# Kernel tuning notes

Hardware: AMD Instinct MI355X
Metric: run time of the kernel (lower is better)

The kernel has to match this reference:

```python
import jax, jax.numpy as jnp
import numpy as np

B, T = 64, 64
H = 256
CLIP = 0.2


def _conv(x, W, b, s):
    y = jax.lax.conv_general_dilated(x, W, (s, s), 'VALID',
                                     dimension_numbers=('NHWC', 'HWIO', 'NHWC'))
    return jax.nn.leaky_relu(y + b, negative_slope=0.2)


def _lstm(x, Wk, Wr, b):
    # keras LSTM, gate order i,f,g,o; x: (B,T,256) -> (B,T,256)
    h0 = jnp.zeros((x.shape[0], H), x.dtype)

    def step(carry, xt):
        h, c = carry
        z = xt @ Wk + h @ Wr + b
        i, f, g, o = jnp.split(z, 4, axis=-1)
        c = jax.nn.sigmoid(f) * c + jax.nn.sigmoid(i) * jnp.tanh(g)
        h = jax.nn.sigmoid(o) * jnp.tanh(c)
        return (h, c), h

    _, hs = jax.lax.scan(step, (h0, h0), jnp.swapaxes(x, 0, 1))
    return jnp.swapaxes(hs, 0, 1)


def setup_inputs():
    key = jax.random.key(0)
    ks = jax.random.split(key, 24)
    s = 0.05
    x = jax.random.normal(ks[0], (B, T, 13, 8, 8), jnp.float32)
    a_taken = jax.random.randint(ks[1], (B, T), 0, 36)
    mask = jax.random.randint(ks[2], (B, T, 4096), 0, 2).astype(jnp.int32)
    # taken actions must be legal (mask=1), as in real rollouts
    bi = jnp.repeat(jnp.arange(B), T)
    ti = jnp.tile(jnp.arange(T), B)
    mask = mask.at[bi, ti, a_taken.reshape(-1)].set(1)
    lg_prob_old = -jnp.abs(jax.random.normal(ks[3], (B, T), jnp.float32)) - 1.0
    GAE = jax.random.normal(ks[4], (B, T), jnp.float32)
    old_v_pred = jax.random.normal(ks[5], (B, T), jnp.float32)
    returns = jax.random.normal(ks[6], (B, T), jnp.float32)
    return {
        'x': x, 'mask': mask, 'lg_prob_old': lg_prob_old, 'a_taken': a_taken,
        'GAE': GAE, 'old_v_pred': old_v_pred, 'returns': returns,
        'W1': jax.random.normal(ks[7], (2, 2, 8, 16), jnp.float32) * s,
        'b1': jnp.zeros((16,), jnp.float32),
        'W2': jax.random.normal(ks[8], (2, 2, 16, 32), jnp.float32) * s,
        'b2': jnp.zeros((32,), jnp.float32),
        'W3': jax.random.normal(ks[9], (2, 2, 32, 64), jnp.float32) * s,
        'b3': jnp.zeros((64,), jnp.float32),
        'W4': jax.random.normal(ks[10], (1, 1, 64, 128), jnp.float32) * s,
        'b4': jnp.zeros((128,), jnp.float32),
        'lstm_k': jax.random.normal(ks[11], (256, 1024), jnp.float32) * s,
        'lstm_r': jax.random.normal(ks[12], (256, 1024), jnp.float32) * s,
        'lstm_b': jnp.zeros((1024,), jnp.float32),
        'pir_W': jax.random.normal(ks[13], (256, 36), jnp.float32) * s,
        'pir_b': jnp.zeros((36,), jnp.float32),
        'pim_W': jax.random.normal(ks[14], (256, 4096), jnp.float32) * s,
        'pim_b': jnp.zeros((4096,), jnp.float32),
        'v_W': jax.random.normal(ks[15], (256, 1), jnp.float32) * s,
        'v_b': jnp.zeros((1,), jnp.float32),
    }


def reference(x, mask, lg_prob_old, a_taken, GAE, old_v_pred, returns,
              W1, b1, W2, b2, W3, b3, W4, b4,
              lstm_k, lstm_r, lstm_b, pir_W, pir_b, pim_W, pim_b, v_W, v_b):
    Bn, Tn = x.shape[0], x.shape[1]
    h = x.reshape(Bn * Tn, 13, 8, 8)  # NHWC: H=13, W=8, C=8
    h = _conv(h, W1, b1, 2)  # (BT,6,4,16)
    h = _conv(h, W2, b2, 1)  # (BT,5,3,32)
    h = _conv(h, W3, b3, 2)  # (BT,2,1,64)
    h = _conv(h, W4, b4, 1)  # (BT,2,1,128)
    # keras Flatten(data_format='channels_first') permutes dim1 to last then flattens
    h = jnp.transpose(h, (0, 2, 3, 1)).reshape(Bn, Tn, -1)  # (B,T,256)
    lstm = _lstm(h, lstm_k, lstm_r, lstm_b).reshape(-1, H)  # (BT,256)

    pir = jax.nn.softmax(lstm @ pir_W + pir_b, axis=-1)  # (BT,36)
    maskf = mask.reshape(-1, 4096).astype(jnp.float32)
    pim = jax.nn.softmax(lstm @ pim_W + pim_b, axis=-1) * maskf
    scale = jnp.sum(pim, axis=1, keepdims=True)
    pim = pim / jnp.where(scale > 0, scale, jnp.ones_like(scale))  # (BT,4096)
    vpred = lstm @ v_W + v_b  # (BT,1)

    lg_old = lg_prob_old.reshape(-1)
    a = a_taken.reshape(-1)
    gae = GAE.reshape(-1)
    ovp = old_v_pred.reshape(-1)
    ret = returns.reshape(-1)
    gae = (gae - jnp.mean(gae)) / (jnp.std(gae) + 1e-8)

    t = jnp.arange(a.shape[0])
    p = jnp.where(t % 2 == 0, pir[t, a], pim[t, a])  # alternating heads
    lg_new = jnp.log(p)
    rt = jnp.exp(lg_new - lg_old)
    pg1 = -gae * rt
    pg2 = -gae * jnp.clip(rt, 1.0 - CLIP, 1.0 + CLIP)
    pg_loss = jnp.mean(jnp.maximum(pg1, pg2))

    # faithful to original TF: (BT,1) vpred broadcast against (BT,) -> (BT,BT)
    vpredclipped = ovp + jnp.clip(vpred - ovp, -CLIP, CLIP)
    vf1 = jnp.square(vpred - ret)
    vf2 = jnp.square(vpredclipped - ret)
    vf_loss = 0.5 * jnp.mean(jnp.maximum(vf1, vf2))

    pim_e = pim + (1.0 - maskf)
    entropy = -jnp.sum(pir * jnp.log(pir)) - jnp.sum(pim_e * jnp.log(pim_e))
    loss = pg_loss - entropy + vf_loss
    return (loss, pg_loss, entropy, vf_loss)
```

## Files before the change

### kernel.cpp

```cpp
#include <hip/hip_runtime.h>

typedef unsigned short u16;
typedef unsigned int   u32;

#define BT   4096
#define TSEQ 64
#define NB   64

typedef __attribute__((ext_vector_type(8))) short  short8;
typedef __attribute__((ext_vector_type(4))) float  f32x4;
typedef __attribute__((ext_vector_type(2))) _Float16 h2;

__device__ __forceinline__ float bf(u16 v) {
    u32 u = ((u32)v) << 16;
    return __builtin_bit_cast(float, u);
}
__device__ __forceinline__ u16 f2b(float f) {
    u32 u = __builtin_bit_cast(u32, f);
    return (u16)((u + 0x7fffu + ((u >> 16) & 1u)) >> 16);
}
__device__ __forceinline__ float lrelu(float x) { return x > 0.f ? x : 0.2f * x; }
__device__ __forceinline__ h2 i2h(int v) { return __builtin_bit_cast(h2, v); }
__device__ __forceinline__ float dot2(int hbits, int wbits, float acc) {
#if __has_builtin(__builtin_amdgcn_fdot2)
    return __builtin_amdgcn_fdot2(i2h(hbits), i2h(wbits), acc, false);
#else
    h2 a = i2h(hbits), b = i2h(wbits);
    return acc + (float)a.x * (float)b.x + (float)a.y * (float)b.y;
#endif
}
__device__ __forceinline__ float fsigm(float x) { return 1.f / (1.f + __expf(-x)); }
__device__ __forceinline__ float ftanh(float x) { return 1.f - 2.f / (__expf(2.f * x) + 1.f); }
__device__ __forceinline__ float ldf(const void* p, int i, int f32) {
    return f32 ? ((const float*)p)[i] : bf(((const u16*)p)[i]);
}
__device__ __forceinline__ u16 ldb(const void* p, int i, int f32) {
    return f32 ? f2b(((const float*)p)[i]) : ((const u16*)p)[i];
}

struct PrepPtrs {
    const void *x, *W1, *b1, *W2, *b2, *W3, *b3, *W4, *b4;
    const void *Wr, *Wk, *Wpim, *Wpir, *Wv;
    const u16* probe;
    u16 *featbf, *PF, *PBk, *PBpim, *PBpir;
    float* scal; int* flag;
};

#define PACK_BLKS 776
#define CONV_BLKS 2048

__global__ __launch_bounds__(256) void prep_kernel(PrepPtrs P)
{
    const int bid = blockIdx.x, tid = threadIdx.x;
    const int lane = tid & 63;
    u16 pv = P.probe[2 * lane];
    int e = (pv >> 7) & 0xFF;
    unsigned long long m = __ballot(pv == 0 || (e >= 100 && e <= 130));
    const int f32 = (__popcll(m) < 48) ? 1 : 0;

    if (bid == 0 && tid < 32) { P.scal[tid] = 0.f; if (tid == 0) *P.flag = f32; }

    if (bid < PACK_BLKS) {
        u16 t8[8];
        if (bid < 128) {
            int gid = bid * 256 + tid;
            int col = gid & 1023, oct = gid >> 10;
#pragma unroll
            for (int j = 0; j < 8; j++) {
                float f = ldf(P.Wr, (oct * 8 + j) * 1024 + col, f32);
                _Float16 h = (_Float16)f;
                t8[j] = __builtin_bit_cast(unsigned short, h);
            }
            *(int4*)&P.PF[((size_t)oct * 1024 + col) * 8] = *(int4*)t8;
        } else if (bid < 256) {
            int gid = (bid - 128) * 256 + tid;
            int col = gid & 1023, oct = gid >> 10;
#pragma unroll
            for (int j = 0; j < 8; j++) t8[j] = ldb(P.Wk, (oct * 8 + j) * 1024 + col, f32);
            *(int4*)&P.PBk[((((size_t)(oct >> 2) << 10) + col) * 4 + (oct & 3)) * 8] = *(int4*)t8;
        } else if (bid < 768) {
            int gid = (bid - 256) * 256 + tid;
            int col = gid & 4095, oct = gid >> 12;
#pragma unroll
            for (int j = 0; j < 8; j++) t8[j] = ldb(P.Wpim, (size_t)(oct * 8 + j) * 4096 + col, f32);
            *(int4*)&P.PBpim[((((size_t)(oct >> 2) << 12) + col) * 4 + (oct & 3)) * 8] = *(int4*)t8;
        } else {
            int gid = (bid - 768) * 256 + tid;
            int col = gid & 63, oct = gid >> 6;
#pragma unroll
            for (int j = 0; j < 8; j++) {
                int k = oct * 8 + j;
                u16 v = 0;
                if (col < 36)       v = ldb(P.Wpir, k * 36 + col, f32);
                else if (col == 36) v = ldb(P.Wv, k, f32);
                t8[j] = v;
            }
            *(int4*)&P.PBpir[(((size_t)(oct >> 2) * 64 + col) * 4 + (oct & 3)) * 8] = *(int4*)t8;
        }
        return;
    }

    __shared__ __align__(16) u16 wl[19184];
    __shared__ float xs[2][832];
    __shared__ float c1[2][384];
    __shared__ float c2[2][480];
    __shared__ float c3[2][128];
    const int pair = bid - PACK_BLKS;
    const int sub = tid >> 7, stid = tid & 127;
    const int bt = pair * 2 + sub;

    {
        const void* sp[8] = {P.W1, P.b1, P.W2, P.b2, P.W3, P.b3, P.W4, P.b4};
        const int   sn[8] = {512, 16, 2048, 32, 8192, 64, 8192, 128};
        int o = 0;
        for (int s = 0; s < 8; s++) {
            for (int i = tid; i < sn[s]; i += 256) wl[o + i] = ldb(sp[s], i, f32);
            o += sn[s];
        }
    }
    for (int i = stid; i < 832; i += 128) xs[sub][i] = ldf(P.x, bt * 832 + i, f32);
    __syncthreads();

    for (int idx = stid; idx < 96; idx += 128) {
        int pos = idx >> 2, g = idx & 3;
        int oh = pos >> 2, ow = pos & 3;
        float a0 = bf(wl[512 + g * 4]), a1 = bf(wl[513 + g * 4]),
              a2 = bf(wl[514 + g * 4]), a3 = bf(wl[515 + g * 4]);
        for (int kh = 0; kh < 2; kh++)
            for (int kw = 0; kw < 2; kw++)
#pragma unroll
                for (int ic = 0; ic < 8; ic++) {
                    float xv = xs[sub][(2 * oh + kh) * 64 + (2 * ow + kw) * 8 + ic];
                    ushort4 w = *(const ushort4*)&wl[((kh * 2 + kw) * 8 + ic) * 16 + g * 4];
                    a0 += xv * bf(w.x); a1 += xv * bf(w.y);
                    a2 += xv * bf(w.z); a3 += xv * bf(w.w);
                }
        c1[sub][pos * 16 + g * 4]     = lrelu(a0);
        c1[sub][pos * 16 + g * 4 + 1] = lrelu(a1);
        c1[sub][pos * 16 + g * 4 + 2] = lrelu(a2);
        c1[sub][pos * 16 + g * 4 + 3] = lrelu(a3);
    }
    __syncthreads();

    for (int idx = stid; idx < 120; idx += 128) {
        int pos = idx >> 3, g = idx & 7;
        int oh = pos / 3, ow = pos % 3;
        float a0 = bf(wl[2576 + g * 4]), a1 = bf(wl[2577 + g * 4]),
              a2 = bf(wl[2578 + g * 4]), a3 = bf(wl[2579 + g * 4]);
        for (int kh = 0; kh < 2; kh++)
            for (int kw = 0; kw < 2; kw++)
#pragma unroll
                for (int ic = 0; ic < 16; ic++) {
                    float xv = c1[sub][((oh + kh) * 4 + (ow + kw)) * 16 + ic];
                    ushort4 w = *(const ushort4*)&wl[528 + ((kh * 2 + kw) * 16 + ic) * 32 + g * 4];
                    a0 += xv * bf(w.x); a1 += xv * bf(w.y);
                    a2 += xv * bf(w.z); a3 += xv * bf(w.w);
                }
        c2[sub][pos * 32 + g * 4]     = lrelu(a0);
        c2[sub][pos * 32 + g * 4 + 1] = lrelu(a1);
        c2[sub][pos * 32 + g * 4 + 2] = lrelu(a2);
        c2[sub][pos * 32 + g * 4 + 3] = lrelu(a3);
    }
    __syncthreads();

    for (int idx = stid; idx < 32; idx += 128) {
        int oh = idx >> 4, g = idx & 15;
        float a0 = bf(wl[10800 + g * 4]), a1 = bf(wl[10801 + g * 4]),
              a2 = bf(wl[10802 + g * 4]), a3 = bf(wl[10803 + g * 4]);
        for (int kh = 0; kh < 2; kh++)
            for (int kw = 0; kw < 2; kw++)
#pragma unroll
                for (int ic = 0; ic < 32; ic++) {
                    float xv = c2[sub][((2 * oh + kh) * 3 + kw) * 32 + ic];
                    ushort4 w = *(const ushort4*)&wl[2608 + ((kh * 2 + kw) * 32 + ic) * 64 + g * 4];
                    a0 += xv * bf(w.x); a1 += xv * bf(w.y);
                    a2 += xv * bf(w.z); a3 += xv * bf(w.w);
                }
        c3[sub][oh * 64 + g * 4]     = lrelu(a0);
        c3[sub][oh * 64 + g * 4 + 1] = lrelu(a1);
        c3[sub][oh * 64 + g * 4 + 2] = lrelu(a2);
        c3[sub][oh * 64 + g * 4 + 3] = lrelu(a3);
    }
    __syncthreads();

    for (int idx = stid; idx < 64; idx += 128) {
        int oh = idx >> 5, g = idx & 31;
        float a0 = bf(wl[19056 + g * 4]), a1 = bf(wl[19057 + g * 4]),
              a2 = bf(wl[19058 + g * 4]), a3 = bf(wl[19059 + g * 4]);
#pragma unroll
        for (int ic = 0; ic < 64; ic++) {
            float xv = c3[sub][oh * 64 + ic];
            ushort4 w = *(const ushort4*)&wl[10864 + ic * 128 + g * 4];
            a0 += xv * bf(w.x); a1 += xv * bf(w.y);
            a2 += xv * bf(w.z); a3 += xv * bf(w.w);
        }
        P.featbf[bt * 256 + (g * 4 + 0) * 2 + oh] = f2b(lrelu(a0));
        P.featbf[bt * 256 + (g * 4 + 1) * 2 + oh] = f2b(lrelu(a1));
        P.featbf[bt * 256 + (g * 4 + 2) * 2 + oh] = f2b(lrelu(a2));
        P.featbf[bt * 256 + (g * 4 + 3) * 2 + oh] = f2b(lrelu(a3));
    }
}

__global__ __launch_bounds__(256) void gemm_zx(
    const u16* __restrict__ Abf, const u16* __restrict__ PB,
    const void* __restrict__ bias, const int* __restrict__ flag,
    float* __restrict__ out)
{
    __shared__ __align__(16) u16 As[16 * 264];
    const int mb = blockIdx.y, nb = blockIdx.x, tid = threadIdx.x;
    const int f32 = *flag;
    const int m0 = mb * 16;
    {
        int row = tid >> 4, part = tid & 15;
        const f32x4* src = (const f32x4*)&Abf[(size_t)(m0 + row) * 256 + part * 16];
        f32x4 v0 = src[0], v1 = src[1];
        *(f32x4*)&As[row * 264 + part * 16] = v0;
        *(f32x4*)&As[row * 264 + part * 16 + 8] = v1;
    }
    __syncthreads();
    const int wv = tid >> 6, lane = tid & 63;
    const int colw = lane & 15, q = lane >> 4;
    const int n = nb * 64 + wv * 16 + colw;
    f32x4 acc = {0.f, 0.f, 0.f, 0.f};
#pragma unroll
    for (int kt = 0; kt < 8; kt++) {
        short8 a = *(const short8*)&As[colw * 264 + kt * 32 + q * 8];
        short8 b = *(const short8*)&PB[((((size_t)kt << 10) + n) * 4 + q) * 8];
        acc = __builtin_amdgcn_mfma_f32_16x16x32_bf16(a, b, acc, 0, 0, 0);
    }
    const float bj = ldf(bias, n, f32);
#pragma unroll
    for (int r = 0; r < 4; r++) {
        int row = q * 4 + r;
        out[(size_t)(m0 + row) * 1024 + n] = acc[r] + bj;
    }
}

#define NREG 12
#define NLDS4 4
__global__ __launch_bounds__(512)
__attribute__((amdgpu_waves_per_eu(2, 2)))
void lstm_kernel(
    const float* __restrict__ zx, const u16* __restrict__ PF,
    u16* __restrict__ hseqbf)
{
    __shared__ __align__(16) u16 h16[264];
    __shared__ __align__(16) float zp[2048];
    __shared__ __align__(16) int4 wlds[2][NLDS4][4][256];
    const int b = blockIdx.x, tid = threadIdx.x;
    const int c = tid & 255, kh = tid >> 8;
    const int4* Pw = (const int4*)PF;

    int4 wr[NREG][4];
#pragma unroll
    for (int o = 0; o < NREG; o++)
#pragma unroll
        for (int g = 0; g < 4; g++)
            wr[o][g] = Pw[(size_t)(kh * 16 + o) * 1024 + g * 256 + c];
#pragma unroll
    for (int o = 0; o < NLDS4; o++)
#pragma unroll
        for (int g = 0; g < 4; g++)
            wlds[kh][o][g][c] = Pw[(size_t)(kh * 16 + NREG + o) * 1024 + g * 256 + c];

    if (tid < 132) ((u32*)h16)[tid] = 0u;
    float cst = 0.f;
    const size_t z0 = (size_t)b * TSEQ * 1024;
    float zxv0 = 0.f, zxv1 = 0.f, zxv2 = 0.f, zxv3 = 0.f;
    if (tid < 256) {
        zxv0 = zx[z0 + c];       zxv1 = zx[z0 + 256 + c];
        zxv2 = zx[z0 + 512 + c]; zxv3 = zx[z0 + 768 + c];
    }
    __syncthreads();

    for (int t = 0; t < TSEQ; t++) {
        float a0 = 0.f, a1 = 0.f, a2 = 0.f, a3 = 0.f;
#pragma unroll
        for (int o = 0; o < NREG; o++) {
            int4 hv = *(const int4*)&h16[(kh * 16 + o) * 8];
            a0 = dot2(hv.x, wr[o][0].x, a0); a0 = dot2(hv.y, wr[o][0].y, a0);
            a0 = dot2(hv.z, wr[o][0].z, a0); a0 = dot2(hv.w, wr[o][0].w, a0);
            a1 = dot2(hv.x, wr[o][1].x, a1); a1 = dot2(hv.y, wr[o][1].y, a1);
            a1 = dot2(hv.z, wr[o][1].z, a1); a1 = dot2(hv.w, wr[o][1].w, a1);
            a2 = dot2(hv.x, wr[o][2].x, a2); a2 = dot2(hv.y, wr[o][2].y, a2);
            a2 = dot2(hv.z, wr[o][2].z, a2); a2 = dot2(hv.w, wr[o][2].w, a2);
            a3 = dot2(hv.x, wr[o][3].x, a3); a3 = dot2(hv.y, wr[o][3].y, a3);
            a3 = dot2(hv.z, wr[o][3].z, a3); a3 = dot2(hv.w, wr[o][3].w, a3);
        }
#pragma unroll
        for (int o = 0; o < NLDS4; o++) {
            int4 hv = *(const int4*)&h16[(kh * 16 + NREG + o) * 8];
            int4 w0 = wlds[kh][o][0][c];
            int4 w1 = wlds[kh][o][1][c];
            int4 w2 = wlds[kh][o][2][c];
            int4 w3 = wlds[kh][o][3][c];
            a0 = dot2(hv.x, w0.x, a0); a0 = dot2(hv.y, w0.y, a0);
            a0 = dot2(hv.z, w0.z, a0); a0 = dot2(hv.w, w0.w, a0);
            a1 = dot2(hv.x, w1.x, a1); a1 = dot2(hv.y, w1.y, a1);
            a1 = dot2(hv.z, w1.z, a1); a1 = dot2(hv.w, w1.w, a1);
            a2 = dot2(hv.x, w2.x, a2); a2 = dot2(hv.y, w2.y, a2);
            a2 = dot2(hv.z, w2.z, a2); a2 = dot2(hv.w, w2.w, a2);
            a3 = dot2(hv.x, w3.x, a3); a3 = dot2(hv.y, w3.y, a3);
            a3 = dot2(hv.z, w3.z, a3); a3 = dot2(hv.w, w3.w, a3);
        }
        *(f32x4*)&zp[((kh << 8) + c) * 4] = (f32x4){a0, a1, a2, a3};
        __syncthreads();

        if (tid < 256) {
            f32x4 s0 = *(const f32x4*)&zp[c * 4];
            f32x4 s1 = *(const f32x4*)&zp[1024 + c * 4];
            float zi = s0.x + s1.x + zxv0;
            float zf = s0.y + s1.y + zxv1;
            float zg = s0.z + s1.z + zxv2;
            float zo = s0.w + s1.w + zxv3;
            if (t + 1 < TSEQ) {
                const size_t zr = z0 + (size_t)(t + 1) * 1024;
                zxv0 = zx[zr + c];       zxv1 = zx[zr + 256 + c];
                zxv2 = zx[zr + 512 + c]; zxv3 = zx[zr + 768 + c];
            }
            float ig = fsigm(zi), fg = fsigm(zf), og = fsigm(zo);
            float gg = ftanh(zg);
            cst = fg * cst + ig * gg;
            float h = og * ftanh(cst);
            h16[c] = __builtin_bit_cast(unsigned short, (_Float16)h);
            hseqbf[(size_t)b * (TSEQ * 256) + t * 256 + c] = f2b(h);
        }
        __syncthreads();
    }
}

__global__ __launch_bounds__(256) void pir_kernel(
    const u16* __restrict__ Abf, const u16* __restrict__ PB,
    const void* __restrict__ pir_b, const void* __restrict__ v_b,
    const int* __restrict__ flag, const int* __restrict__ a_taken,
    float* __restrict__ entpir, float* __restrict__ ppira, float* __restrict__ vpred)
{
    __shared__ __align__(16) u16 As[64 * 264];
    const int tid = threadIdx.x;
    const int wv = tid >> 6, lane = tid & 63;
    const int colw = lane & 15, q = lane >> 4;
    const int f32 = *flag;
    const int m0 = blockIdx.x * 64;

    for (int idx = tid; idx < 1024; idx += 256) {
        int row = idx >> 4, part = idx & 15;
        const f32x4* src = (const f32x4*)&Abf[(size_t)(m0 + row) * 256 + part * 16];
        f32x4 v0 = src[0], v1 = src[1];
        *(f32x4*)&As[row * 264 + part * 16] = v0;
        *(f32x4*)&As[row * 264 + part * 16 + 8] = v1;
    }
    __syncthreads();
    f32x4 acc[4];
#pragma unroll
    for (int nt = 0; nt < 4; nt++) acc[nt] = (f32x4){0.f, 0.f, 0.f, 0.f};
#pragma unroll
    for (int kt = 0; kt < 8; kt++) {
        short8 a = *(const short8*)&As[(wv * 16 + colw) * 264 + kt * 32 + q * 8];
#pragma unroll
        for (int nt = 0; nt < 4; nt++) {
            short8 b = *(const short8*)&PB[((((size_t)kt * 64) + nt * 16 + colw) * 4 + q) * 8];
            acc[nt] = __builtin_amdgcn_mfma_f32_16x16x32_bf16(a, b, acc[nt], 0, 0, 0);
        }
    }
    float* zq = (float*)&As[wv * 4224];
#pragma unroll
    for (int nt = 0; nt < 4; nt++) {
        int col = nt * 16 + colw;
        float bj = (col < 36) ? ldf(pir_b, col, f32)
                              : (col == 36 ? ldf(v_b, 0, f32) : 0.f);
#pragma unroll
        for (int r = 0; r < 4; r++)
            zq[(q * 4 + r) * 65 + col] = acc[nt][r] + bj;
    }
    if (lane < 16) {
        int R = m0 + wv * 16 + lane;
        const float* zrow = &zq[lane * 65];
        float Z = 0.f, U = 0.f;
        for (int cc = 0; cc < 36; cc++) {
            float z = zrow[cc];
            float ev = __expf(z);
            Z += ev; U += ev * z;
        }
        entpir[R] = logf(Z) - U / Z;
        ppira[R]  = __expf(zrow[a_taken[R]]) / Z;
        vpred[R]  = zrow[36];
    }
}

__global__ __launch_bounds__(256) void pim_kernel(
    const u16* __restrict__ Abf, const u16* __restrict__ PB,
    const void* __restrict__ pim_b, const int* __restrict__ flag,
    const int* __restrict__ mask, const int* __restrict__ a_taken,
    float* __restrict__ partS, float* __restrict__ partU, float* __restrict__ za)
{
    __shared__ __align__(16) u16 As[32 * 264];
    __shared__ float redS[4][32], redU[4][32];
    const int nb = blockIdx.x, mb = blockIdx.y, tid = threadIdx.x;
    const int wv = tid >> 6, lane = tid & 63;
    const int colw = lane & 15, q = lane >> 4;
    const int f32 = *flag;
    const int m0 = mb * 32;

    for (int idx = tid; idx < 512; idx += 256) {
        int row = idx >> 4, part = idx & 15;
        const f32x4* src = (const f32x4*)&Abf[(size_t)(m0 + row) * 256 + part * 16];
        f32x4 v0 = src[0], v1 = src[1];
        *(f32x4*)&As[row * 264 + part * 16] = v0;
        *(f32x4*)&As[row * 264 + part * 16 + 8] = v1;
    }
    __syncthreads();
    const int n = nb * 64 + wv * 16 + colw;
    f32x4 acc0 = {0.f, 0.f, 0.f, 0.f}, acc1 = {0.f, 0.f, 0.f, 0.f};
#pragma unroll
    for (int kt = 0; kt < 8; kt++) {
        short8 b = *(const short8*)&PB[((((size_t)kt << 12) + n) * 4 + q) * 8];
        short8 a0 = *(const short8*)&As[colw * 264 + kt * 32 + q * 8];
        short8 a1 = *(const short8*)&As[(16 + colw) * 264 + kt * 32 + q * 8];
        acc0 = __builtin_amdgcn_mfma_f32_16x16x32_bf16(a0, b, acc0, 0, 0, 0);
        acc1 = __builtin_amdgcn_mfma_f32_16x16x32_bf16(a1, b, acc1, 0, 0, 0);
    }
    const float bj = ldf(pim_b, n, f32);
#pragma unroll
    for (int half = 0; half < 2; half++) {
        const f32x4& acc = half ? acc1 : acc0;
        float sv[4], uv[4];
#pragma unroll
        for (int r = 0; r < 4; r++) {
            int row = m0 + half * 16 + q * 4 + r;
            float z = acc[r] + bj;
            int mm = mask[(size_t)row * 4096 + n];
            float ev = __expf(z);
            sv[r] = mm ? ev : 0.f;
            uv[r] = mm ? ev * z : 0.f;
            if (n == a_taken[row]) za[row] = z;
        }
#pragma unroll
        for (int r = 0; r < 4; r++) {
            for (int off = 1; off < 16; off <<= 1) {
                sv[r] += __shfl_xor(sv[r], off, 16);
                uv[r] += __shfl_xor(uv[r], off, 16);
            }
            if (colw == 0) {
                redS[wv][half * 16 + q * 4 + r] = sv[r];
                redU[wv][half * 16 + q * 4 + r] = uv[r];
            }
        }
    }
    __syncthreads();
    if (tid < 32) {
        float S = redS[0][tid] + redS[1][tid] + redS[2][tid] + redS[3][tid];
        float U = redU[0][tid] + redU[1][tid] + redU[2][tid] + redU[3][tid];
        partS[(size_t)(m0 + tid) * 64 + nb] = S;
        partU[(size_t)(m0 + tid) * 64 + nb] = U;
    }
}

#define TAIL_BLOCKS (16 + 256)
__global__ __launch_bounds__(256) void tail_kernel(
    const float* __restrict__ partS, const float* __restrict__ partU,
    const float* __restrict__ za,
    const float* __restrict__ entpir, const float* __restrict__ ppira,
    const float* __restrict__ vpred,
    const void* __restrict__ lgold, const void* __restrict__ gae,
    const void* __restrict__ ovp, const void* __restrict__ ret,
    float* __restrict__ scal, const int* __restrict__ flag,
    void* __restrict__ out)
{
    const int bid = blockIdx.x, tid = threadIdx.x;
    const int f32 = *flag;
    __shared__ float sh[8];
    __shared__ float mst[2];
    if (bid < 16) {
        const int r = bid * 256 + tid;
        float S = 0.f, U = 0.f;
#pragma unroll
        for (int t2 = 0; t2 < 64; t2++) {
            S += partS[(size_t)r * 64 + t2];
            U += partU[(size_t)r * 64 + t2];
        }
        float entpim = logf(S) - U / S;
        float ppima = __expf(za[r]) / S;
        float s = 0.f, s2 = 0.f;
        if (f32) {
            const float* gp = (const float*)gae;
            for (int i = tid; i < BT; i += 256) { float v = gp[i]; s += v; s2 += v * v; }
        } else {
            const u16* gp = (const u16*)gae;
            for (int i = tid; i < BT; i += 256) { float v = bf(gp[i]); s += v; s2 += v * v; }
        }
        for (int off = 32; off; off >>= 1) {
            s += __shfl_down(s, off, 64); s2 += __shfl_down(s2, off, 64);
        }
        if ((tid & 63) == 0) { sh[tid >> 6] = s; sh[4 + (tid >> 6)] = s2; }
        __syncthreads();
        if (tid == 0) {
            float Sa = sh[0] + sh[1] + sh[2] + sh[3];
            float S2a = sh[4] + sh[5] + sh[6] + sh[7];
            float mean = Sa / (float)BT;
            float var = S2a / (float)BT - mean * mean;
            mst[0] = mean; mst[1] = sqrtf(fmaxf(var, 0.f));
        }
        __syncthreads();
        float mean = mst[0], sd = mst[1];
        float p = (r & 1) ? ppima : ppira[r];
        float ln = logf(p);
        float rt = __expf(ln - ldf(lgold, r, f32));
        float g = (ldf(gae, r, f32) - mean) / (sd + 1e-8f);
        float rtc = fminf(fmaxf(rt, 0.8f), 1.2f);
        float pg = fmaxf(-g * rt, -g * rtc);
        float e12 = entpir[r] + entpim;
        for (int off = 32; off; off >>= 1) {
            pg += __shfl_down(pg, off, 64);
            e12 += __shfl_down(e12, off, 64);
        }
        if ((tid & 63) == 0) {
            atomicAdd(&scal[2], pg);
            atomicAdd(&scal[3], e12);
        }
    } else {
        const int i0 = (bid - 16) * 16;
        float s = 0.f;
        if (f32) {
            const float* rp = (const float*)ret;
            const float* op = (const float*)ovp;
            for (int rr = 0; rr < 16; rr++) {
                float vp = vpred[i0 + rr];
                for (int j = tid; j < BT; j += 256) {
                    float r2 = rp[j], o = op[j];
                    float d = fminf(fmaxf(vp - o, -0.2f), 0.2f);
                    float v1 = vp - r2;    v1 *= v1;
                    float v2 = o + d - r2; v2 *= v2;
                    s += fmaxf(v1, v2);
                }
            }
        } else {
            const u16* rp = (const u16*)ret;
            const u16* op = (const u16*)ovp;
            for (int rr = 0; rr < 16; rr++) {
                float vp = vpred[i0 + rr];
                for (int j = tid; j < BT; j += 256) {
                    float r2 = bf(rp[j]), o = bf(op[j]);
                    float d = fminf(fmaxf(vp - o, -0.2f), 0.2f);
                    float v1 = vp - r2;    v1 *= v1;
                    float v2 = o + d - r2; v2 *= v2;
                    s += fmaxf(v1, v2);
                }
            }
        }
        for (int off = 32; off; off >>= 1) s += __shfl_down(s, off, 64);
        if ((tid & 63) == 0) sh[tid >> 6] = s;
        __syncthreads();
        if (tid == 0) atomicAdd(&scal[5], sh[0] + sh[1] + sh[2] + sh[3]);
    }
    __threadfence();
    __syncthreads();
    if (tid == 0) {
        unsigned old = atomicAdd((unsigned int*)&scal[8], 1u);
        if (old == TAIL_BLOCKS - 1) {
            __threadfence();
            float pgs = atomicAdd(&scal[2], 0.f);
            float ents = atomicAdd(&scal[3], 0.f);
            float vfs = atomicAdd(&scal[5], 0.f);
            float pg = pgs / (float)BT;
            float vf = 0.5f * vfs / ((float)BT * (float)BT);
            float loss = pg - ents + vf;
            if (f32) {
                float* o = (float*)out;
                o[0] = loss; o[1] = pg; o[2] = ents; o[3] = vf;
            } else {
                u16* o = (u16*)out;
                o[0] = f2b(loss); o[1] = f2b(pg); o[2] = f2b(ents); o[3] = f2b(vf);
            }
        }
    }
}

extern "C" void kernel_launch(void* const* d_in, const int* in_sizes, int n_in,
                              void* d_out, int out_size, void* d_ws, size_t ws_size,
                              hipStream_t stream)
{
    const int* mask = (const int*)d_in[1];
    const int* a_tk = (const int*)d_in[3];

    float* p = (float*)d_ws;
    u16*   featbf = (u16*)p;            p += 524288;
    float* zx     = p;                  p += 4194304;
    u16*   hseqbf = (u16*)p;            p += 524288;
    u16*   PF     = (u16*)p;            p += 131072;
    u16*   PBk    = (u16*)p;            p += 131072;
    u16*   PBpim  = (u16*)p;            p += 524288;
    u16*   PBpir  = (u16*)p;            p += 8192;
    float* scal   = p;                  p += 32;
    int*   flag   = (int*)p;            p += 4;
    float* partS  = p;                  p += 262144;
    float* partU  = p;                  p += 262144;
    float* za     = p;                  p += 4096;
    float* entpir = p;                  p += 4096;
    float* ppira  = p;                  p += 4096;
    float* vpred  = p;                  p += 4096;

    PrepPtrs P;
    P.x = d_in[0];
    P.W1 = d_in[7];  P.b1 = d_in[8];
    P.W2 = d_in[9];  P.b2 = d_in[10];
    P.W3 = d_in[11]; P.b3 = d_in[12];
    P.W4 = d_in[13]; P.b4 = d_in[14];
    P.Wk = d_in[15]; P.Wr = d_in[16];
    P.Wpir = d_in[18]; P.Wpim = d_in[20]; P.Wv = d_in[22];
    P.probe = (const u16*)d_in[15];
    P.featbf = featbf; P.PF = PF; P.PBk = PBk; P.PBpim = PBpim; P.PBpir = PBpir;
    P.scal = scal; P.flag = flag;

    prep_kernel<<<PACK_BLKS + CONV_BLKS, 256, 0, stream>>>(P);
    gemm_zx<<<dim3(16, 256), 256, 0, stream>>>(featbf, PBk, d_in[17], flag, zx);
    lstm_kernel<<<NB, 512, 0, stream>>>(zx, PF, hseqbf);
    pir_kernel<<<64, 256, 0, stream>>>(hseqbf, PBpir, d_in[19], d_in[23], flag,
                                       a_tk, entpir, ppira, vpred);
    pim_kernel<<<dim3(64, 128), 256, 0, stream>>>(hseqbf, PBpim, d_in[21], flag,
                                                  mask, a_tk, partS, partU, za);
    tail_kernel<<<TAIL_BLOCKS, 256, 0, stream>>>(
        partS, partU, za, entpir, ppira, vpred,
        d_in[2], d_in[4], d_in[5], d_in[6], scal, flag, (void*)d_out);
}
```

Measured before the change: 454.7 us.

## Broadcast LSTM hidden state via readlane and force register weight loads with asm

The LSTM recurrence now loads the hidden state once per lane from LDS and broadcasts each chunk to the wave with readlane, replacing repeated uniform LDS vector reads. The register-resident weights are loaded with inline global_load_dwordx4 asm so the compiler keeps them in VGPRs instead of spilling or rematerialising. The prep kernel's weight staging is vectorised to float4 or int4 loads. Readlane moves work to scalar registers and may serialise, and the asm waitcnt stalls on each group of four loads.

```diff
diff --git a/kernel.cpp b/kernel.cpp
--- a/kernel.cpp
+++ b/kernel.cpp
@@ -9,6 +9,7 @@
 
 typedef __attribute__((ext_vector_type(8))) short  short8;
 typedef __attribute__((ext_vector_type(4))) float  f32x4;
+typedef __attribute__((ext_vector_type(4))) int    i32x4;
 typedef __attribute__((ext_vector_type(2))) _Float16 h2;
 
 __device__ __forceinline__ float bf(u16 v) {
@@ -38,6 +39,20 @@
     return f32 ? f2b(((const float*)p)[i]) : ((const u16*)p)[i];
 }
 
+__device__ __forceinline__ void gload4x4(const void* p0, const void* p1,
+                                         const void* p2, const void* p3,
+                                         i32x4& r0, i32x4& r1, i32x4& r2, i32x4& r3)
+{
+    asm volatile("global_load_dwordx4 %0, %4, off\n\t"
+                 "global_load_dwordx4 %1, %5, off\n\t"
+                 "global_load_dwordx4 %2, %6, off\n\t"
+                 "global_load_dwordx4 %3, %7, off\n\t"
+                 "s_waitcnt vmcnt(0)"
+                 : "=&v"(r0), "=&v"(r1), "=&v"(r2), "=&v"(r3)
+                 : "v"(p0), "v"(p1), "v"(p2), "v"(p3)
+                 : "memory");
+}
+
 struct PrepPtrs {
     const void *x, *W1, *b1, *W2, *b2, *W3, *b3, *W4, *b4;
     const void *Wr, *Wk, *Wpim, *Wpir, *Wv;
@@ -114,7 +129,19 @@
         const int   sn[8] = {512, 16, 2048, 32, 8192, 64, 8192, 128};
         int o = 0;
         for (int s = 0; s < 8; s++) {
-            for (int i = tid; i < sn[s]; i += 256) wl[o + i] = ldb(sp[s], i, f32);
+            if (f32) {
+                const float4* src = (const float4*)sp[s];
+                for (int i = tid; i < (sn[s] >> 2); i += 256) {
+                    float4 v = src[i];
+                    ushort4 w;
+                    w.x = f2b(v.x); w.y = f2b(v.y); w.z = f2b(v.z); w.w = f2b(v.w);
+                    *(ushort4*)&wl[o + i * 4] = w;
+                }
+            } else {
+                const int4* src = (const int4*)sp[s];
+                for (int i = tid; i < (sn[s] >> 3); i += 256)
+                    *(int4*)&wl[o + i * 8] = src[i];
+            }
             o += sn[s];
         }
     }
@@ -249,19 +276,24 @@
     __shared__ __align__(16) int4 wlds[2][NLDS4][4][256];
     const int b = blockIdx.x, tid = threadIdx.x;
     const int c = tid & 255, kh = tid >> 8;
-    const int4* Pw = (const int4*)PF;
-
-    int4 wr[NREG][4];
-#pragma unroll
-    for (int o = 0; o < NREG; o++)
-#pragma unroll
-        for (int g = 0; g < 4; g++)
-            wr[o][g] = Pw[(size_t)(kh * 16 + o) * 1024 + g * 256 + c];
-#pragma unroll
-    for (int o = 0; o < NLDS4; o++)
-#pragma unroll
-        for (int g = 0; g < 4; g++)
-            wlds[kh][o][g][c] = Pw[(size_t)(kh * 16 + NREG + o) * 1024 + g * 256 + c];
+
+    i32x4 wr[NREG][4];
+#pragma unroll
+    for (int o = 0; o < NREG; o++) {
+        const u16* p0 = &PF[((size_t)(kh * 16 + o) * 1024 + 0 * 256 + c) * 8];
+        const u16* p1 = &PF[((size_t)(kh * 16 + o) * 1024 + 1 * 256 + c) * 8];
+        const u16* p2 = &PF[((size_t)(kh * 16 + o) * 1024 + 2 * 256 + c) * 8];
+        const u16* p3 = &PF[((size_t)(kh * 16 + o) * 1024 + 3 * 256 + c) * 8];
+        gload4x4(p0, p1, p2, p3, wr[o][0], wr[o][1], wr[o][2], wr[o][3]);
+    }
+    {
+        const int4* Pw = (const int4*)PF;
+#pragma unroll
+        for (int o = 0; o < NLDS4; o++)
+#pragma unroll
+            for (int g = 0; g < 4; g++)
+                wlds[kh][o][g][c] = Pw[(size_t)(kh * 16 + NREG + o) * 1024 + g * 256 + c];
+    }
 
     if (tid < 132) ((u32*)h16)[tid] = 0u;
     float cst = 0.f;
@@ -274,34 +306,42 @@
     __syncthreads();
 
     for (int t = 0; t < TSEQ; t++) {
+        int4 vh = *(const int4*)&h16[(kh * 16 + (tid & 15)) * 8];
         float a0 = 0.f, a1 = 0.f, a2 = 0.f, a3 = 0.f;
 #pragma unroll
-        for (int o = 0; o < NREG; o++) {
-            int4 hv = *(const int4*)&h16[(kh * 16 + o) * 8];
-            a0 = dot2(hv.x, wr[o][0].x, a0); a0 = dot2(hv.y, wr[o][0].y, a0);
-            a0 = dot2(hv.z, wr[o][0].z, a0); a0 = dot2(hv.w, wr[o][0].w, a0);
-            a1 = dot2(hv.x, wr[o][1].x, a1); a1 = dot2(hv.y, wr[o][1].y, a1);
-            a1 = dot2(hv.z, wr[o][1].z, a1); a1 = dot2(hv.w, wr[o][1].w, a1);
-            a2 = dot2(hv.x, wr[o][2].x, a2); a2 = dot2(hv.y, wr[o][2].y, a2);
-            a2 = dot2(hv.z, wr[o][2].z, a2); a2 = dot2(hv.w, wr[o][2].w, a2);
-            a3 = dot2(hv.x, wr[o][3].x, a3); a3 = dot2(hv.y, wr[o][3].y, a3);
-            a3 = dot2(hv.z, wr[o][3].z, a3); a3 = dot2(hv.w, wr[o][3].w, a3);
-        }
-#pragma unroll
-        for (int o = 0; o < NLDS4; o++) {
-            int4 hv = *(const int4*)&h16[(kh * 16 + NREG + o) * 8];
-            int4 w0 = wlds[kh][o][0][c];
-            int4 w1 = wlds[kh][o][1][c];
-            int4 w2 = wlds[kh][o][2][c];
-            int4 w3 = wlds[kh][o][3][c];
-            a0 = dot2(hv.x, w0.x, a0); a0 = dot2(hv.y, w0.y, a0);
-            a0 = dot2(hv.z, w0.z, a0); a0 = dot2(hv.w, w0.w, a0);
-            a1 = dot2(hv.x, w1.x, a1); a1 = dot2(hv.y, w1.y, a1);
-            a1 = dot2(hv.z, w1.z, a1); a1 = dot2(hv.w, w1.w, a1);
-            a2 = dot2(hv.x, w2.x, a2); a2 = dot2(hv.y, w2.y, a2);
-            a2 = dot2(hv.z, w2.z, a2); a2 = dot2(hv.w, w2.w, a2);
-            a3 = dot2(hv.x, w3.x, a3); a3 = dot2(hv.y, w3.y, a3);
-            a3 = dot2(hv.z, w3.z, a3); a3 = dot2(hv.w, w3.w, a3);
+        for (int j = 0; j < NREG; j++) {
+            int h0 = __builtin_amdgcn_readlane(vh.x, j);
+            int h1 = __builtin_amdgcn_readlane(vh.y, j);
+            int h2 = __builtin_amdgcn_readlane(vh.z, j);
+            int h3 = __builtin_amdgcn_readlane(vh.w, j);
+            a0 = dot2(h0, wr[j][0].x, a0); a0 = dot2(h1, wr[j][0].y, a0);
+            a0 = dot2(h2, wr[j][0].z, a0); a0 = dot2(h3, wr[j][0].w, a0);
+            a1 = dot2(h0, wr[j][1].x, a1); a1 = dot2(h1, wr[j][1].y, a1);
+            a1 = dot2(h2, wr[j][1].z, a1); a1 = dot2(h3, wr[j][1].w, a1);
+            a2 = dot2(h0, wr[j][2].x, a2); a2 = dot2(h1, wr[j][2].y, a2);
+            a2 = dot2(h2, wr[j][2].z, a2); a2 = dot2(h3, wr[j][2].w, a2);
+            a3 = dot2(h0, wr[j][3].x, a3); a3 = dot2(h1, wr[j][3].y, a3);
+            a3 = dot2(h2, wr[j][3].z, a3); a3 = dot2(h3, wr[j][3].w, a3);
+        }
+#pragma unroll
+        for (int jj = 0; jj < NLDS4; jj++) {
+            const int j = NREG + jj;
+            int4 w0 = wlds[kh][jj][0][c];
+            int4 w1 = wlds[kh][jj][1][c];
+            int4 w2 = wlds[kh][jj][2][c];
+            int4 w3 = wlds[kh][jj][3][c];
+            int h0 = __builtin_amdgcn_readlane(vh.x, j);
+            int h1 = __builtin_amdgcn_readlane(vh.y, j);
+            int h2 = __builtin_amdgcn_readlane(vh.z, j);
+            int h3 = __builtin_amdgcn_readlane(vh.w, j);
+            a0 = dot2(h0, w0.x, a0); a0 = dot2(h1, w0.y, a0);
+            a0 = dot2(h2, w0.z, a0); a0 = dot2(h3, w0.w, a0);
+            a1 = dot2(h0, w1.x, a1); a1 = dot2(h1, w1.y, a1);
+            a1 = dot2(h2, w1.z, a1); a1 = dot2(h3, w1.w, a1);
+            a2 = dot2(h0, w2.x, a2); a2 = dot2(h1, w2.y, a2);
+            a2 = dot2(h2, w2.z, a2); a2 = dot2(h3, w2.w, a2);
+            a3 = dot2(h0, w3.x, a3); a3 = dot2(h1, w3.y, a3);
+            a3 = dot2(h2, w3.z, a3); a3 = dot2(h3, w3.w, a3);
         }
         *(f32x4*)&zp[((kh << 8) + c) * 4] = (f32x4){a0, a1, a2, a3};
         __syncthreads();
```

After: 427.0 us. 6.1% less time.

## Pair LSTM K-halves in adjacent lanes, reduce via shuffle, double-buffer h

Applied to the files above, without the earlier changes.

The LSTM step now maps the two K-halves of each hidden unit to adjacent lanes and combines their partial gate sums with a cross-lane shuffle. This removes the shared-memory partial-sum buffer and one of the two block barriers per timestep. The hidden state is double-buffered so the next step's reads do not race with the current step's writes, and all 512 threads now compute the gate math redundantly. Separately, the conv weight staging loads weights with vectorized float4/int4 reads instead of scalar loads.

```diff
diff --git a/kernel.cpp b/kernel.cpp
--- a/kernel.cpp
+++ b/kernel.cpp
@@ -9,6 +9,7 @@
 
 typedef __attribute__((ext_vector_type(8))) short  short8;
 typedef __attribute__((ext_vector_type(4))) float  f32x4;
+typedef __attribute__((ext_vector_type(4))) int    i32x4;
 typedef __attribute__((ext_vector_type(2))) _Float16 h2;
 
 __device__ __forceinline__ float bf(u16 v) {
@@ -114,7 +115,19 @@
         const int   sn[8] = {512, 16, 2048, 32, 8192, 64, 8192, 128};
         int o = 0;
         for (int s = 0; s < 8; s++) {
-            for (int i = tid; i < sn[s]; i += 256) wl[o + i] = ldb(sp[s], i, f32);
+            if (f32) {
+                const float4* src = (const float4*)sp[s];
+                for (int i = tid; i < (sn[s] >> 2); i += 256) {
+                    float4 v = src[i];
+                    ushort4 w;
+                    w.x = f2b(v.x); w.y = f2b(v.y); w.z = f2b(v.z); w.w = f2b(v.w);
+                    *(ushort4*)&wl[o + i * 4] = w;
+                }
+            } else {
+                const int4* src = (const int4*)sp[s];
+                for (int i = tid; i < (sn[s] >> 3); i += 256)
+                    *(int4*)&wl[o + i * 8] = src[i];
+            }
             o += sn[s];
         }
     }
@@ -244,11 +257,10 @@
     const float* __restrict__ zx, const u16* __restrict__ PF,
     u16* __restrict__ hseqbf)
 {
-    __shared__ __align__(16) u16 h16[264];
-    __shared__ __align__(16) float zp[2048];
+    __shared__ __align__(16) u16 h16[2][264];
     __shared__ __align__(16) int4 wlds[2][NLDS4][4][256];
     const int b = blockIdx.x, tid = threadIdx.x;
-    const int c = tid & 255, kh = tid >> 8;
+    const int c = tid >> 1, kh = tid & 1;
     const int4* Pw = (const int4*)PF;
 
     int4 wr[NREG][4];
@@ -263,21 +275,19 @@
         for (int g = 0; g < 4; g++)
             wlds[kh][o][g][c] = Pw[(size_t)(kh * 16 + NREG + o) * 1024 + g * 256 + c];
 
-    if (tid < 132) ((u32*)h16)[tid] = 0u;
+    if (tid < 128) ((u32*)h16[0])[tid] = 0u;
     float cst = 0.f;
     const size_t z0 = (size_t)b * TSEQ * 1024;
-    float zxv0 = 0.f, zxv1 = 0.f, zxv2 = 0.f, zxv3 = 0.f;
-    if (tid < 256) {
-        zxv0 = zx[z0 + c];       zxv1 = zx[z0 + 256 + c];
-        zxv2 = zx[z0 + 512 + c]; zxv3 = zx[z0 + 768 + c];
-    }
+    float zxv0 = zx[z0 + c],       zxv1 = zx[z0 + 256 + c];
+    float zxv2 = zx[z0 + 512 + c], zxv3 = zx[z0 + 768 + c];
     __syncthreads();
 
     for (int t = 0; t < TSEQ; t++) {
+        const u16* hb = h16[t & 1];
         float a0 = 0.f, a1 = 0.f, a2 = 0.f, a3 = 0.f;
 #pragma unroll
         for (int o = 0; o < NREG; o++) {
-            int4 hv = *(const int4*)&h16[(kh * 16 + o) * 8];
+            int4 hv = *(const int4*)&hb[(kh * 16 + o) * 8];
             a0 = dot2(hv.x, wr[o][0].x, a0); a0 = dot2(hv.y, wr[o][0].y, a0);
             a0 = dot2(hv.z, wr[o][0].z, a0); a0 = dot2(hv.w, wr[o][0].w, a0);
             a1 = dot2(hv.x, wr[o][1].x, a1); a1 = dot2(hv.y, wr[o][1].y, a1);
@@ -289,7 +299,7 @@
         }
 #pragma unroll
         for (int o = 0; o < NLDS4; o++) {
-            int4 hv = *(const int4*)&h16[(kh * 16 + NREG + o) * 8];
+            int4 hv = *(const int4*)&hb[(kh * 16 + NREG + o) * 8];
             int4 w0 = wlds[kh][o][0][c];
             int4 w1 = wlds[kh][o][1][c];
             int4 w2 = wlds[kh][o][2][c];
@@ -303,28 +313,21 @@
             a3 = dot2(hv.x, w3.x, a3); a3 = dot2(hv.y, w3.y, a3);
             a3 = dot2(hv.z, w3.z, a3); a3 = dot2(hv.w, w3.w, a3);
         }
-        *(f32x4*)&zp[((kh << 8) + c) * 4] = (f32x4){a0, a1, a2, a3};
-        __syncthreads();
-
-        if (tid < 256) {
-            f32x4 s0 = *(const f32x4*)&zp[c * 4];
-            f32x4 s1 = *(const f32x4*)&zp[1024 + c * 4];
-            float zi = s0.x + s1.x + zxv0;
-            float zf = s0.y + s1.y + zxv1;
-            float zg = s0.z + s1.z + zxv2;
-            float zo = s0.w + s1.w + zxv3;
-            if (t + 1 < TSEQ) {
-                const size_t zr = z0 + (size_t)(t + 1) * 1024;
-                zxv0 = zx[zr + c];       zxv1 = zx[zr + 256 + c];
-                zxv2 = zx[zr + 512 + c]; zxv3 = zx[zr + 768 + c];
-            }
-            float ig = fsigm(zi), fg = fsigm(zf), og = fsigm(zo);
-            float gg = ftanh(zg);
-            cst = fg * cst + ig * gg;
-            float h = og * ftanh(cst);
-            h16[c] = __builtin_bit_cast(unsigned short, (_Float16)h);
-            hseqbf[(size_t)b * (TSEQ * 256) + t * 256 + c] = f2b(h);
-        }
+        float zi = a0 + __shfl_xor(a0, 1, 64) + zxv0;
+        float zf = a1 + __shfl_xor(a1, 1, 64) + zxv1;
+        float zg = a2 + __shfl_xor(a2, 1, 64) + zxv2;
+        float zo = a3 + __shfl_xor(a3, 1, 64) + zxv3;
+        if (t + 1 < TSEQ) {
+            const size_t zr = z0 + (size_t)(t + 1) * 1024;
+            zxv0 = zx[zr + c];       zxv1 = zx[zr + 256 + c];
+            zxv2 = zx[zr + 512 + c]; zxv3 = zx[zr + 768 + c];
+        }
+        float ig = fsigm(zi), fg = fsigm(zf), og = fsigm(zo);
+        float gg = ftanh(zg);
+        cst = fg * cst + ig * gg;
+        float h = og * ftanh(cst);
+        if (kh == 0) h16[(t & 1) ^ 1][c] = __builtin_bit_cast(unsigned short, (_Float16)h);
+        else         hseqbf[(size_t)b * (TSEQ * 256) + t * 256 + c] = f2b(h);
         __syncthreads();
     }
 }
```

Measured after the change: 435.1 us. -4.3%, faster.
